# Optimization experiments

Hardware: AMD Instinct MI355X
Metric: run time of the kernel (lower is better)

## Reference

```python
import jax, jax.numpy as jnp
import numpy as np

N, P, D = 128, 256, 256
H, M = 16, 32            # num_heads, head_dim; output_dim = H*M = 512
OUT, HID = H * M, 2048


def setup_inputs() -> dict:
    key = jax.random.key(0)
    ks = jax.random.split(key, 7)
    s = 0.02
    return {
        "x": jax.random.normal(ks[0], (N, P, D), jnp.float32),
        "qkv_temporal": jax.random.normal(ks[1], (3, D, H, M), jnp.float32) * s,
        "qkv_point": jax.random.normal(ks[2], (3, H, M, H, M), jnp.float32) * s,
        "W1": jax.random.normal(ks[3], (OUT, HID), jnp.float32) * s,
        "b1": jnp.zeros((HID,), jnp.float32),
        "W2": jax.random.normal(ks[4], (HID, OUT), jnp.float32) * s,
        "b2": jnp.zeros((OUT,), jnp.float32),
    }


def reference(x, qkv_temporal, qkv_point, W1, b1, W2, b2):
    # ---- temporal attention (over frames i/I, per point j) ----
    qkv = jnp.einsum('wdhm,ijd->whmij', qkv_temporal, x)     # (3,H,M,N,P)
    q, k, v = qkv[0], qkv[1], qkv[2]
    scores = jnp.einsum('hmij,hmIj->hiIj', q, k)             # (H,N,N,P)
    weights = jax.nn.softmax(scores, axis=2)
    # NOTE: label order 'hIij' (positional) matches the original source exactly
    temporal = jnp.einsum('hIij,hmIj->hmij', weights, v)     # (H,M,N,P)
    # ---- point attention (over points j/J, per frame i) ----
    qkv = jnp.einsum('whmHM,HMij->whmij', qkv_point, temporal)  # (3,H,M,N,P)
    q, k, v = qkv[0], qkv[1], qkv[2]
    scores = jnp.einsum('hmij,hmiJ->hijJ', q, k)             # (H,N,P,P)
    weights = jax.nn.softmax(scores, axis=-1)
    pa = jnp.einsum('hijJ,hmiJ->ijhm', weights, v)           # (N,P,H,M)
    pa = pa.reshape(pa.shape[0], pa.shape[1], -1)            # (N,P,H*M)
    # ---- two-layer MLP (no activation, matching the source) ----
    h = pa @ W1 + b1
    return h @ W2 + b2
```

## Files before the change

### kernel.cpp

```cpp
#include <hip/hip_runtime.h>
#include <cstddef>
#include <cstdint>

constexpr int Nf = 128, Pp = 256, Dd = 256, Hh = 16, Mm = 32;
constexpr int OUTC = 512, HID = 2048, C3 = 1536;

typedef short short8 __attribute__((ext_vector_type(8)));
typedef float f32x4 __attribute__((ext_vector_type(4)));

__device__ inline unsigned short f2bf(float f) {
  unsigned u = __float_as_uint(f);
  u += 0x7fffu + ((u >> 16) & 1u);
  return (unsigned short)(u >> 16);
}
__device__ inline unsigned pk2(float a, float b) {
  return (unsigned)f2bf(a) | ((unsigned)f2bf(b) << 16);
}

__global__ __launch_bounds__(256) void conv_x(const float* __restrict__ x,
                                              short* __restrict__ xb) {
  int idx = blockIdx.x * 256 + threadIdx.x;
  const float4* s = (const float4*)x + (size_t)idx * 2;
  float4 a = s[0], c = s[1];
  uint4 o;
  o.x = pk2(a.x, a.y); o.y = pk2(a.z, a.w);
  o.z = pk2(c.x, c.y); o.w = pk2(c.z, c.w);
  ((uint4*)xb)[idx] = o;
}

__global__ __launch_bounds__(256) void transpose_to_bf16(const float* __restrict__ in,
                                                         short* __restrict__ out,
                                                         int R, int C) {
  __shared__ float tile[64 * 65];
  const int t = threadIdx.x;
  const int rb = blockIdx.y * 64, cb = blockIdx.x * 64;
  const size_t sl = (size_t)blockIdx.z * R * C;
#pragma unroll
  for (int u = 0; u < 4; ++u) {
    int r = (t >> 4) + u * 16, c4 = (t & 15) * 4;
    float4 v = *(const float4*)(in + sl + (size_t)(rb + r) * C + cb + c4);
    tile[r * 65 + c4 + 0] = v.x;
    tile[r * 65 + c4 + 1] = v.y;
    tile[r * 65 + c4 + 2] = v.z;
    tile[r * 65 + c4 + 3] = v.w;
  }
  __syncthreads();
#pragma unroll
  for (int u = 0; u < 2; ++u) {
    int id = t + u * 256;
    int n = id >> 3, kg = id & 7;
    float a[8];
#pragma unroll
    for (int q = 0; q < 8; ++q) a[q] = tile[(kg * 8 + q) * 65 + n];
    uint4 o;
    o.x = pk2(a[0], a[1]); o.y = pk2(a[2], a[3]);
    o.z = pk2(a[4], a[5]); o.w = pk2(a[6], a[7]);
    *(uint4*)(out + sl + (size_t)(cb + n) * R + rb + kg * 8) = o;
  }
}

__global__ void repack_b2t(const float* __restrict__ Wp, short* __restrict__ B2t) {
  int idx = blockIdx.x * 256 + threadIdx.x;
  int c = idx >> 9, k = idx & 511;
  int w = c >> 9, h = (c >> 5) & 15, m = c & 31;
  int HH = k >> 5, MM = k & 31;
  B2t[idx] = (short)f2bf(Wp[(((w * Hh + h) * Mm + m) * Hh + HH) * Mm + MM]);
}

__global__ __launch_bounds__(256) void wc_splitk(const short* __restrict__ A,
                                                 const short* __restrict__ Bt,
                                                 float* __restrict__ part) {
  __shared__ short As[128 * 32];
  __shared__ short Bs[128 * 32];
  const int t = threadIdx.x;
  const int wv = t >> 6, ln = t & 63;
  const int wr = wv >> 1, wc = wv & 1;
  const int lr = ln & 15, kq = ln >> 4;
  const int row0 = blockIdx.y * 128, col0 = blockIdx.x * 128;
  const int k0 = blockIdx.z * 256;

  f32x4 acc[4][4];
#pragma unroll
  for (int i = 0; i < 4; ++i)
#pragma unroll
    for (int j = 0; j < 4; ++j) acc[i][j] = {0.f, 0.f, 0.f, 0.f};

  for (int kt = k0; kt < k0 + 256; kt += 32) {
#pragma unroll
    for (int u = 0; u < 2; ++u) {
      int seg = wv * 128 + u * 64 + ln;
      int r = seg >> 2, kg = seg & 3;
      const short* gp = A + (size_t)(row0 + r) * HID + kt + kg * 8;
      __builtin_amdgcn_global_load_lds(
          (const __attribute__((address_space(1))) void*)gp,
          (__attribute__((address_space(3))) void*)&As[(wv * 128 + u * 64) * 8], 16, 0, 0);
    }
#pragma unroll
    for (int u = 0; u < 2; ++u) {
      int seg = wv * 128 + u * 64 + ln;
      int r = seg >> 2, kg = seg & 3;
      const short* gp = Bt + (size_t)(col0 + r) * HID + kt + kg * 8;
      __builtin_amdgcn_global_load_lds(
          (const __attribute__((address_space(1))) void*)gp,
          (__attribute__((address_space(3))) void*)&Bs[(wv * 128 + u * 64) * 8], 16, 0, 0);
    }
    __syncthreads();
    short8 a[4], b[4];
#pragma unroll
    for (int ti = 0; ti < 4; ++ti)
      a[ti] = *(const short8*)&As[(wr * 64 + ti * 16 + lr) * 32 + kq * 8];
#pragma unroll
    for (int tj = 0; tj < 4; ++tj)
      b[tj] = *(const short8*)&Bs[(wc * 64 + tj * 16 + lr) * 32 + kq * 8];
#pragma unroll
    for (int ti = 0; ti < 4; ++ti)
#pragma unroll
      for (int tj = 0; tj < 4; ++tj)
        acc[ti][tj] = __builtin_amdgcn_mfma_f32_16x16x32_bf16(a[ti], b[tj], acc[ti][tj], 0, 0, 0);
    __syncthreads();
  }

#pragma unroll
  for (int tj = 0; tj < 4; ++tj) {
    int gcol = col0 + wc * 64 + tj * 16 + lr;
#pragma unroll
    for (int ti = 0; ti < 4; ++ti)
#pragma unroll
      for (int rg = 0; rg < 4; ++rg) {
        int grow = row0 + wr * 64 + ti * 16 + kq * 4 + rg;
        part[((size_t)blockIdx.z * 512 + grow) * 512 + gcol] = acc[ti][tj][rg];
      }
  }
}

__global__ __launch_bounds__(256) void wc_reduce(const float* __restrict__ part,
                                                 short* __restrict__ Wct) {
  int idx = blockIdx.x * 256 + threadIdx.x;
  float s = 0.f;
#pragma unroll
  for (int z = 0; z < 8; ++z) s += part[(size_t)z * 262144 + idx];
  Wct[idx] = (short)f2bf(s);
}

__global__ __launch_bounds__(256) void bc_partial(const float* __restrict__ b1,
                                                  const float* __restrict__ W2,
                                                  float* __restrict__ part) {
  const int z = blockIdx.x;
  const int t = threadIdx.x;
  float s0 = 0.f, s1 = 0.f;
#pragma unroll
  for (int hh = 0; hh < 32; ++hh) {
    int h = z * 32 + hh;
    float bv = b1[h];
    s0 += bv * W2[(size_t)h * OUTC + t];
    s1 += bv * W2[(size_t)h * OUTC + t + 256];
  }
  part[z * OUTC + t] = s0;
  part[z * OUTC + t + 256] = s1;
}

__global__ __launch_bounds__(256) void bc_finish(const float* __restrict__ part,
                                                 const float* __restrict__ b2,
                                                 float* __restrict__ bc) {
  int o = blockIdx.x * 256 + threadIdx.x;
  float s = b2[o];
#pragma unroll
  for (int z = 0; z < 64; ++z) s += part[z * OUTC + o];
  bc[o] = s;
}

template <int KDIM, int NCOLS, int AMAP, int EPI, int OUTT>
__global__ __launch_bounds__(256) void gemm_mfma(const short* __restrict__ A,
                                                 const short* __restrict__ Bt,
                                                 void* __restrict__ Cv,
                                                 const float* __restrict__ bias,
                                                 int j0, int pshift, int pc) {
  __shared__ __align__(16) short SH[16384];
  const int t = threadIdx.x;
  const int wv = t >> 6, ln = t & 63;
  const int wr = wv >> 1, wc = wv & 1;
  const int lr = ln & 15, kq = ln >> 4;

  constexpr int NBX = NCOLS / 128;
  constexpr int NT = KDIM / 32;
  int lin = blockIdx.y * NBX + blockIdx.x;
  int nblk = gridDim.x * gridDim.y;
  int bx, by;
  if ((nblk & 7) == 0) {
    int per = nblk >> 3;
    int id = (lin & 7) * per + (lin >> 3);
    bx = id % NBX; by = id / NBX;
  } else {
    bx = blockIdx.x; by = blockIdx.y;
  }
  const int row0 = by * 128, col0 = bx * 128;

  const int seg0 = wv * 128 + ln;
  const int seg1 = wv * 128 + 64 + ln;
  const int r0 = seg0 >> 2, r1 = seg1 >> 2;
  const int kg0 = (seg0 & 3) ^ ((r0 >> 1) & 3);
  const int kg1 = (seg1 & 3) ^ ((r1 >> 1) & 3);
  size_t arow0, arow1;
  {
    int rr = row0 + r0;
    if (AMAP == 0)      arow0 = (size_t)rr;
    else if (AMAP == 3) arow0 = (size_t)(((rr & 127) << 8) + (rr >> 7));
    else { int i = rr >> pshift, jj = rr & (pc - 1); arow0 = (size_t)((i << 8) + j0 + jj); }
    rr = row0 + r1;
    if (AMAP == 0)      arow1 = (size_t)rr;
    else if (AMAP == 3) arow1 = (size_t)(((rr & 127) << 8) + (rr >> 7));
    else { int i = rr >> pshift, jj = rr & (pc - 1); arow1 = (size_t)((i << 8) + j0 + jj); }
  }
  const size_t brow0 = (size_t)(col0 + r0), brow1 = (size_t)(col0 + r1);

  auto stage = [&](int buf, int tk) {
    const int kt = tk * 32;
    __builtin_amdgcn_global_load_lds(
        (const __attribute__((address_space(1))) void*)(A + arow0 * KDIM + kt + kg0 * 8),
        (__attribute__((address_space(3))) void*)&SH[buf * 4096 + (wv * 128) * 8], 16, 0, 0);
    __builtin_amdgcn_global_load_lds(
        (const __attribute__((address_space(1))) void*)(A + arow1 * KDIM + kt + kg1 * 8),
        (__attribute__((address_space(3))) void*)&SH[buf * 4096 + (wv * 128 + 64) * 8], 16, 0, 0);
    __builtin_amdgcn_global_load_lds(
        (const __attribute__((address_space(1))) void*)(Bt + brow0 * KDIM + kt + kg0 * 8),
        (__attribute__((address_space(3))) void*)&SH[8192 + buf * 4096 + (wv * 128) * 8], 16, 0, 0);
    __builtin_amdgcn_global_load_lds(
        (const __attribute__((address_space(1))) void*)(Bt + brow1 * KDIM + kt + kg1 * 8),
        (__attribute__((address_space(3))) void*)&SH[8192 + buf * 4096 + (wv * 128 + 64) * 8], 16, 0, 0);
  };

  f32x4 acc[4][4];
#pragma unroll
  for (int i = 0; i < 4; ++i)
#pragma unroll
    for (int j = 0; j < 4; ++j) acc[i][j] = {0.f, 0.f, 0.f, 0.f};

  const int slot = kq ^ ((lr >> 1) & 3);

  stage(0, 0);
  stage(1, 1);
  asm volatile("s_waitcnt vmcnt(4)" ::: "memory");
  __builtin_amdgcn_s_barrier();

  for (int tk = 0; tk < NT; ++tk) {
    const int cur = tk & 1;
    short8 a[4], b[4];
#pragma unroll
    for (int ti = 0; ti < 4; ++ti)
      a[ti] = *(const short8*)&SH[cur * 4096 + (wr * 64 + ti * 16 + lr) * 32 + slot * 8];
#pragma unroll
    for (int tj = 0; tj < 4; ++tj)
      b[tj] = *(const short8*)&SH[8192 + cur * 4096 + (wc * 64 + tj * 16 + lr) * 32 + slot * 8];
    __builtin_amdgcn_sched_barrier(0);
    asm volatile("s_waitcnt lgkmcnt(0)" ::: "memory");
    __builtin_amdgcn_sched_barrier(0);
    if (tk + 1 < NT) {
      __builtin_amdgcn_s_barrier();
      if (tk + 2 < NT) stage(cur, tk + 2);
    }
#pragma unroll
    for (int ti = 0; ti < 4; ++ti)
#pragma unroll
      for (int tj = 0; tj < 4; ++tj)
        acc[ti][tj] = __builtin_amdgcn_mfma_f32_16x16x32_bf16(a[ti], b[tj], acc[ti][tj], 0, 0, 0);
    if (tk + 1 < NT) {
      if (tk + 2 < NT) {
        asm volatile("s_waitcnt vmcnt(4)" ::: "memory");
      } else {
        asm volatile("s_waitcnt vmcnt(0)" ::: "memory");
      }
      __builtin_amdgcn_s_barrier();
      __builtin_amdgcn_sched_barrier(0);
    }
  }

  if (EPI == 0 || EPI == 1) {
#pragma unroll
    for (int tj = 0; tj < 4; ++tj) {
      int gcol = col0 + wc * 64 + tj * 16 + lr;
      float bv = (EPI == 0) ? bias[gcol] : 0.f;
#pragma unroll
      for (int ti = 0; ti < 4; ++ti) {
#pragma unroll
        for (int rg = 0; rg < 4; ++rg) {
          int grow = row0 + wr * 64 + ti * 16 + kq * 4 + rg;
          float val = acc[ti][tj][rg];
          if (EPI == 0) {
            val += bv;
            if (OUTT == 0) ((short*)Cv)[(size_t)grow * NCOLS + gcol] = (short)f2bf(val);
            else           ((float*)Cv)[(size_t)grow * NCOLS + gcol] = val;
          } else {
            int w = gcol >> 9, h = (gcol >> 5) & 15, m = gcol & 31;
            int i = grow >> pshift, jj = grow & (pc - 1);
            size_t addr = (((size_t)(w * Hh + h) * pc + jj) * Nf + i) * Mm + m;
            ((short*)Cv)[addr] = (short)f2bf(val);
          }
        }
      }
    }
  } else {
    __builtin_amdgcn_s_barrier();
#pragma unroll
    for (int ti = 0; ti < 4; ++ti)
#pragma unroll
      for (int tj = 0; tj < 4; ++tj) {
        int c = wc * 64 + tj * 16 + lr;
        int q = c >> 5, m = c & 31;
#pragma unroll
        for (int rg = 0; rg < 4; ++rg) {
          int g = wr * 64 + ti * 16 + kq * 4 + rg;
          SH[q * 4096 + g * 32 + (m ^ ((g & 4) << 2))] = (short)f2bf(acc[ti][tj][rg]);
        }
      }
    __syncthreads();
#pragma unroll
    for (int u = 0; u < 8; ++u) {
      int id = u * 256 + t;
      int q = id >> 9, rem = id & 511, g = rem >> 2, mc = (rem & 3) * 8;
      uint4 v = *(const uint4*)&SH[q * 4096 + g * 32 + (mc ^ ((g & 4) << 2))];
      int gc = col0 + q * 32;
      int w = gc >> 9, h = (gc >> 5) & 15;
      size_t base;
      if (EPI == 3) base = ((size_t)(w * Hh + h) * 256 + (row0 >> 7)) * 4096;
      else          base = (((size_t)(w * Hh + h) * pc + (row0 >> 8)) * 256 + (row0 & 255)) * 32;
      *(uint4*)((short*)Cv + base + g * 32 + mc) = v;
    }
  }
}

__global__ __launch_bounds__(256) void temporal_attn_mfma(const short* __restrict__ T,
                                                          short* __restrict__ At,
                                                          int j0, int jcShift) {
  constexpr int QsO = 0, KsO = 4096, VtO = 8192, WtO = 12544, RsO = 29952;
  __shared__ __align__(16) short lds[30464];
  float* rs = (float*)&lds[RsO];
  const int JC = 1 << jcShift;
  const int h  = blockIdx.x >> jcShift;
  const int jj = blockIdx.x & (JC - 1);
  const int t  = threadIdx.x;
  const int wv = t >> 6, ln = t & 63;
  const int wr = wv >> 1, wc = wv & 1;
  const int lr = ln & 15, kq = ln >> 4;
  const size_t WC = (size_t)(Hh << jcShift) * 4096;
  const short* qb = T + (size_t)(h * JC + jj) * 4096;
  const short* kb = qb + WC;
  const short* vb = qb + 2 * WC;

#pragma unroll
  for (int u = 0; u < 2; ++u) {
    int seg = wv * 2 + u;
    __builtin_amdgcn_global_load_lds(
        (const __attribute__((address_space(1))) void*)(qb + seg * 512 + ln * 8),
        (__attribute__((address_space(3))) void*)&lds[QsO + seg * 512], 16, 0, 0);
    __builtin_amdgcn_global_load_lds(
        (const __attribute__((address_space(1))) void*)(kb + seg * 512 + ln * 8),
        (__attribute__((address_space(3))) void*)&lds[KsO + seg * 512], 16, 0, 0);
  }
#pragma unroll
  for (int u = 0; u < 2; ++u) {
    int idx = t + u * 256;
    int I = idx >> 2, m0 = (idx & 3) * 8;
    uint4 v = *(const uint4*)(vb + idx * 8);
    const short* vs = (const short*)&v;
#pragma unroll
    for (int q = 0; q < 8; ++q) lds[VtO + (m0 + q) * 136 + I] = vs[q];
  }
  __syncthreads();

  short8 af[4], bf[4];
#pragma unroll
  for (int ti = 0; ti < 4; ++ti)
    af[ti] = *(const short8*)&lds[QsO + (wr * 64 + ti * 16 + lr) * 32 + kq * 8];
#pragma unroll
  for (int tj = 0; tj < 4; ++tj)
    bf[tj] = *(const short8*)&lds[KsO + (wc * 64 + tj * 16 + lr) * 32 + kq * 8];
  f32x4 e[4][4];
#pragma unroll
  for (int ti = 0; ti < 4; ++ti)
#pragma unroll
    for (int tj = 0; tj < 4; ++tj) e[ti][tj] = {0.f, 0.f, 0.f, 0.f};
#pragma unroll
  for (int ti = 0; ti < 4; ++ti)
#pragma unroll
    for (int tj = 0; tj < 4; ++tj)
      e[ti][tj] = __builtin_amdgcn_mfma_f32_16x16x32_bf16(af[ti], bf[tj], e[ti][tj], 0, 0, 0);

  float part[4][4];
#pragma unroll
  for (int ti = 0; ti < 4; ++ti)
#pragma unroll
    for (int r = 0; r < 4; ++r) {
      float p = 0.f;
#pragma unroll
      for (int tj = 0; tj < 4; ++tj) {
        float ex = __expf(e[ti][tj][r]);
        e[ti][tj][r] = ex;
        p += ex;
      }
      part[ti][r] = p;
    }
#pragma unroll
  for (int msk = 1; msk <= 8; msk <<= 1)
#pragma unroll
    for (int ti = 0; ti < 4; ++ti)
#pragma unroll
      for (int r = 0; r < 4; ++r)
        part[ti][r] += __shfl_xor(part[ti][r], msk, 64);
  if (lr == 0) {
#pragma unroll
    for (int ti = 0; ti < 4; ++ti)
#pragma unroll
      for (int r = 0; r < 4; ++r)
        rs[wc * 128 + wr * 64 + ti * 16 + kq * 4 + r] = part[ti][r];
  }
  __syncthreads();

#pragma unroll
  for (int ti = 0; ti < 4; ++ti) {
#pragma unroll
    for (int r = 0; r < 4; ++r) {
      int I = wr * 64 + ti * 16 + kq * 4 + r;
      float inv = 1.f / (rs[I] + rs[128 + I]);
#pragma unroll
      for (int tj = 0; tj < 4; ++tj) e[ti][tj][r] *= inv;
    }
#pragma unroll
    for (int tj = 0; tj < 4; ++tj) {
      int i = wc * 64 + tj * 16 + lr;
      int Ib = wr * 64 + ti * 16 + kq * 4;
      uint2 pk;
      pk.x = pk2(e[ti][tj][0], e[ti][tj][1]);
      pk.y = pk2(e[ti][tj][2], e[ti][tj][3]);
      *(uint2*)&lds[WtO + i * 136 + Ib] = pk;
    }
  }
  __syncthreads();

  f32x4 o[2][2];
#pragma unroll
  for (int tr = 0; tr < 2; ++tr)
#pragma unroll
    for (int tm = 0; tm < 2; ++tm) o[tr][tm] = {0.f, 0.f, 0.f, 0.f};
#pragma unroll
  for (int ks = 0; ks < 4; ++ks) {
    short8 ea[2], vf[2];
#pragma unroll
    for (int tr = 0; tr < 2; ++tr)
      ea[tr] = *(const short8*)&lds[WtO + (wv * 32 + tr * 16 + lr) * 136 + ks * 32 + kq * 8];
#pragma unroll
    for (int tm = 0; tm < 2; ++tm)
      vf[tm] = *(const short8*)&lds[VtO + (tm * 16 + lr) * 136 + ks * 32 + kq * 8];
#pragma unroll
    for (int tr = 0; tr < 2; ++tr)
#pragma unroll
      for (int tm = 0; tm < 2; ++tm)
        o[tr][tm] = __builtin_amdgcn_mfma_f32_16x16x32_bf16(ea[tr], vf[tm], o[tr][tm], 0, 0, 0);
  }
#pragma unroll
  for (int tr = 0; tr < 2; ++tr)
#pragma unroll
    for (int tm = 0; tm < 2; ++tm)
#pragma unroll
      for (int r = 0; r < 4; ++r) {
        int row = wv * 32 + tr * 16 + kq * 4 + r;
        lds[row * 40 + tm * 16 + lr] = (short)f2bf(o[tr][tm][r]);
      }
  __syncthreads();
#pragma unroll
  for (int u = 0; u < 2; ++u) {
    int idx = t + u * 256;
    int i = idx >> 2, mg = idx & 3;
    uint4 vv = *(const uint4*)&lds[i * 40 + mg * 8];
    *(uint4*)(At + ((size_t)(i * Pp + j0 + jj) * OUTC + h * 32 + mg * 8)) = vv;
  }
}

__global__ __launch_bounds__(256) void point_attn_mfma(const short* __restrict__ P,
                                                       short* __restrict__ PA,
                                                       int icShift) {
  constexpr int QsO = 0, KsO = 4096, VtO = 8192, EO = 12544, CsO = 29952;
  __shared__ __align__(16) short lds[30720];
  float* cs    = (float*)&lds[CsO];
  float* denom = cs + 256;
  const int IC = 1 << icShift;
  const int bx = blockIdx.x;
  const int h    = bx >> (icShift + 1);
  const int rem  = bx & ((IC << 1) - 1);
  const int ii   = rem >> 1;
  const int half = rem & 1;
  const int t  = threadIdx.x;
  const int wv = t >> 6, ln = t & 63;
  const int wr = wv >> 1, wc = wv & 1;
  const int lr = ln & 15, kq = ln >> 4;
  const size_t WC = (size_t)(Hh << icShift) * 8192;
  const short* qb = P + (size_t)(h * IC + ii) * 8192 + half * 4096;
  const short* kb = P + WC + (size_t)(h * IC + ii) * 8192;
  const short* vb = kb + WC;

  f32x4 o[2][2];
#pragma unroll
  for (int tr = 0; tr < 2; ++tr)
#pragma unroll
    for (int tm = 0; tm < 2; ++tm) o[tr][tm] = {0.f, 0.f, 0.f, 0.f};

  for (int chunk = 0; chunk < 2; ++chunk) {
    const int Jb = chunk * 128;
    if (chunk) __syncthreads();
#pragma unroll
    for (int u = 0; u < 2; ++u) {
      int seg = wv * 2 + u;
      __builtin_amdgcn_global_load_lds(
          (const __attribute__((address_space(1))) void*)(kb + Jb * 32 + seg * 512 + ln * 8),
          (__attribute__((address_space(3))) void*)&lds[KsO + seg * 512], 16, 0, 0);
    }
    if (chunk == 0) {
#pragma unroll
      for (int u = 0; u < 2; ++u) {
        int seg = wv * 2 + u;
        __builtin_amdgcn_global_load_lds(
            (const __attribute__((address_space(1))) void*)(qb + seg * 512 + ln * 8),
            (__attribute__((address_space(3))) void*)&lds[QsO + seg * 512], 16, 0, 0);
      }
      if (t < 128) denom[t] = 0.f;
    }
#pragma unroll
    for (int u = 0; u < 2; ++u) {
      int idx = t + u * 256;
      int Jl = idx >> 2, m0 = (idx & 3) * 8;
      uint4 v = *(const uint4*)(vb + Jb * 32 + idx * 8);
      const short* vs = (const short*)&v;
#pragma unroll
      for (int q = 0; q < 8; ++q) lds[VtO + (m0 + q) * 136 + Jl] = vs[q];
    }
    __syncthreads();

    short8 af[4], bf[4];
#pragma unroll
    for (int ti = 0; ti < 4; ++ti)
      af[ti] = *(const short8*)&lds[KsO + (wr * 64 + ti * 16 + lr) * 32 + kq * 8];
#pragma unroll
    for (int tj = 0; tj < 4; ++tj)
      bf[tj] = *(const short8*)&lds[QsO + (wc * 64 + tj * 16 + lr) * 32 + kq * 8];
    f32x4 e[4][4];
#pragma unroll
    for (int ti = 0; ti < 4; ++ti)
#pragma unroll
      for (int tj = 0; tj < 4; ++tj) e[ti][tj] = {0.f, 0.f, 0.f, 0.f};
#pragma unroll
    for (int ti = 0; ti < 4; ++ti)
#pragma unroll
      for (int tj = 0; tj < 4; ++tj)
        e[ti][tj] = __builtin_amdgcn_mfma_f32_16x16x32_bf16(af[ti], bf[tj], e[ti][tj], 0, 0, 0);

    float cp[4] = {0.f, 0.f, 0.f, 0.f};
#pragma unroll
    for (int ti = 0; ti < 4; ++ti)
#pragma unroll
      for (int tj = 0; tj < 4; ++tj)
#pragma unroll
        for (int r = 0; r < 4; ++r) {
          float ex = __expf(e[ti][tj][r]);
          e[ti][tj][r] = ex;
          cp[tj] += ex;
        }
#pragma unroll
    for (int tj = 0; tj < 4; ++tj) {
      cp[tj] += __shfl_xor(cp[tj], 16, 64);
      cp[tj] += __shfl_xor(cp[tj], 32, 64);
    }
    if (kq == 0) {
#pragma unroll
      for (int tj = 0; tj < 4; ++tj)
        cs[wr * 128 + wc * 64 + tj * 16 + lr] = cp[tj];
    }
#pragma unroll
    for (int ti = 0; ti < 4; ++ti)
#pragma unroll
      for (int tj = 0; tj < 4; ++tj) {
        int j  = wc * 64 + tj * 16 + lr;
        int Jl = wr * 64 + ti * 16 + kq * 4;
        uint2 pk;
        pk.x = pk2(e[ti][tj][0], e[ti][tj][1]);
        pk.y = pk2(e[ti][tj][2], e[ti][tj][3]);
        *(uint2*)&lds[EO + j * 136 + Jl] = pk;
      }
    __syncthreads();
    if (t < 128) denom[t] += cs[t] + cs[128 + t];

#pragma unroll
    for (int ks = 0; ks < 4; ++ks) {
      short8 ea[2], vf[2];
#pragma unroll
      for (int tr = 0; tr < 2; ++tr)
        ea[tr] = *(const short8*)&lds[EO + (wv * 32 + tr * 16 + lr) * 136 + ks * 32 + kq * 8];
#pragma unroll
      for (int tm = 0; tm < 2; ++tm)
        vf[tm] = *(const short8*)&lds[VtO + (tm * 16 + lr) * 136 + ks * 32 + kq * 8];
#pragma unroll
      for (int tr = 0; tr < 2; ++tr)
#pragma unroll
        for (int tm = 0; tm < 2; ++tm)
          o[tr][tm] = __builtin_amdgcn_mfma_f32_16x16x32_bf16(ea[tr], vf[tm], o[tr][tm], 0, 0, 0);
    }
  }
  __syncthreads();

#pragma unroll
  for (int tr = 0; tr < 2; ++tr)
#pragma unroll
    for (int r = 0; r < 4; ++r) {
      int row = wv * 32 + tr * 16 + kq * 4 + r;
      float rinv = 1.f / denom[row];
#pragma unroll
      for (int tm = 0; tm < 2; ++tm)
        lds[row * 40 + tm * 16 + lr] = (short)f2bf(o[tr][tm][r] * rinv);
    }
  __syncthreads();
#pragma unroll
  for (int u = 0; u < 2; ++u) {
    int idx = t + u * 256;
    int jl = idx >> 2, mg = idx & 3;
    uint4 vv = *(const uint4*)&lds[jl * 40 + mg * 8];
    *(uint4*)(PA + ((size_t)(ii * Pp + half * 128 + jl) * OUTC + h * 32 + mg * 8)) = vv;
  }
}

extern "C" void kernel_launch(void* const* d_in, const int* in_sizes, int n_in,
                              void* d_out, int out_size, void* d_ws, size_t ws_size,
                              hipStream_t stream) {
  const float* x  = (const float*)d_in[0];
  const float* Wt = (const float*)d_in[1];
  const float* Wp = (const float*)d_in[2];
  const float* W1 = (const float*)d_in[3];
  const float* b1 = (const float*)d_in[4];
  const float* W2 = (const float*)d_in[5];
  const float* b2 = (const float*)d_in[6];
  float* out = (float*)d_out;
  short* ws  = (short*)d_ws;

  const size_t fixedH = 8388608 + 16777216 + 393216 + 786432 + 1048576 + 1048576
                      + 262144 + 1024 + 4194304 + 65536;
  size_t availH = ws_size / 2;
  size_t chF; int JC, IC;
  if      (availH >= fixedH + 50331648) { chF = 50331648; JC = 256; IC = 128; }
  else if (availH >= fixedH + 12582912) { chF = 12582912; JC = 64;  IC = 32;  }
  else if (availH >= fixedH + 6291456)  { chF = 6291456;  JC = 32;  IC = 16;  }
  else                                  { chF = 3145728;  JC = 16;  IC = 8;   }
  short* CH  = ws;
  short* xbf = CH + chF;
  short* At  = xbf + 8388608;
  short* B1t = At + 16777216;
  short* B2t = B1t + 393216;
  short* W1b = B2t + 786432;
  short* W2t = W1b + 1048576;
  short* Wct = W2t + 1048576;
  float* bcF   = (float*)(Wct + 262144);
  float* partF = (float*)(Wct + 262144 + 1024);
  float* bcP   = (float*)(Wct + 262144 + 1024 + 4194304);
  const int jcS = __builtin_ctz((unsigned)JC);
  const int icS = __builtin_ctz((unsigned)IC);

  conv_x<<<4096, 256, 0, stream>>>(x, xbf);
  conv_x<<<512, 256, 0, stream>>>(W1, W1b);
  transpose_to_bf16<<<dim3(8, 4, 3), 256, 0, stream>>>(Wt, B1t, 256, 512);
  repack_b2t<<<3072, 256, 0, stream>>>(Wp, B2t);
  transpose_to_bf16<<<dim3(8, 32, 1), 256, 0, stream>>>(W2, W2t, 2048, 512);

  wc_splitk<<<dim3(4, 4, 8), 256, 0, stream>>>(W2t, W1b, partF);
  wc_reduce<<<1024, 256, 0, stream>>>(partF, Wct);
  bc_partial<<<64, 256, 0, stream>>>(b1, W2, bcP);
  bc_finish<<<2, 256, 0, stream>>>(bcP, b2, bcF);

  if (JC == 256) {
    gemm_mfma<256, 1536, 3, 3, 0><<<dim3(12, 256), 256, 0, stream>>>(xbf, B1t, CH, nullptr, 0, 0, 256);
    temporal_attn_mfma<<<Hh * 256, 256, 0, stream>>>(CH, At, 0, 8);
    gemm_mfma<512, 1536, 0, 2, 0><<<dim3(12, 256), 256, 0, stream>>>(At, B2t, CH, nullptr, 0, 0, 128);
    point_attn_mfma<<<Hh * 128 * 2, 256, 0, stream>>>(CH, At, 7);
  } else {
    for (int j0 = 0; j0 < Pp; j0 += JC) {
      gemm_mfma<256, 1536, 1, 1, 0><<<dim3(12, JC), 256, 0, stream>>>(xbf, B1t, CH, nullptr, j0, jcS, JC);
      temporal_attn_mfma<<<Hh * JC, 256, 0, stream>>>(CH, At, j0, jcS);
    }
    for (int i0 = 0; i0 < Nf; i0 += IC) {
      short* Arows = At + (size_t)i0 * Pp * OUTC;
      gemm_mfma<512, 1536, 0, 2, 0><<<dim3(12, IC * 2), 256, 0, stream>>>(Arows, B2t, CH, nullptr, 0, 0, IC);
      point_attn_mfma<<<Hh * IC * 2, 256, 0, stream>>>(CH, Arows, icS);
    }
  }

  gemm_mfma<512, 512, 0, 0, 1><<<dim3(4, 256), 256, 0, stream>>>(At, Wct, out, bcF, 0, 0, 0);
}
```

Before: 368.2 us.

## Swizzle Q/K LDS layout, rotate V transpose stores, use hardware bf16 pack

Q and K tiles are now loaded into LDS with an XOR-swizzled 16-byte slot per row, and the MFMA fragment reads use the matching swizzled slot. The aim is to remove LDS bank conflicts on the short8 reads in both attention kernels. The V transpose stores are rotated per lane group so the four groups write different rows in the same cycle, which targets conflicts in the scattered 2-byte stores. The software float-to-bf16 rounding in pk2 is replaced with the v_cvt_pk_bf16_f32 instruction, which risks small rounding or NaN-handling differences and depends on the instruction being available on this target.

```diff
diff --git a/kernel.cpp b/kernel.cpp
--- a/kernel.cpp
+++ b/kernel.cpp
@@ -14,7 +14,9 @@
   return (unsigned short)(u >> 16);
 }
 __device__ inline unsigned pk2(float a, float b) {
-  return (unsigned)f2bf(a) | ((unsigned)f2bf(b) << 16);
+  unsigned r;
+  asm("v_cvt_pk_bf16_f32 %0, %1, %2" : "=v"(r) : "v"(a), "v"(b));
+  return r;
 }
 
 __global__ __launch_bounds__(256) void conv_x(const float* __restrict__ x,
@@ -346,34 +348,45 @@
   const short* kb = qb + WC;
   const short* vb = qb + 2 * WC;
 
+  const int lnoff = (ln >> 2) * 32 + (((ln & 3) ^ ((ln >> 3) & 3)) * 8);
+  const int qkslot = (kq ^ ((lr >> 1) & 3)) * 8;
+
 #pragma unroll
   for (int u = 0; u < 2; ++u) {
     int seg = wv * 2 + u;
     __builtin_amdgcn_global_load_lds(
-        (const __attribute__((address_space(1))) void*)(qb + seg * 512 + ln * 8),
+        (const __attribute__((address_space(1))) void*)(qb + seg * 512 + lnoff),
         (__attribute__((address_space(3))) void*)&lds[QsO + seg * 512], 16, 0, 0);
     __builtin_amdgcn_global_load_lds(
-        (const __attribute__((address_space(1))) void*)(kb + seg * 512 + ln * 8),
+        (const __attribute__((address_space(1))) void*)(kb + seg * 512 + lnoff),
         (__attribute__((address_space(3))) void*)&lds[KsO + seg * 512], 16, 0, 0);
   }
 #pragma unroll
   for (int u = 0; u < 2; ++u) {
     int idx = t + u * 256;
-    int I = idx >> 2, m0 = (idx & 3) * 8;
+    int I = idx >> 2, g = idx & 3;
     uint4 v = *(const uint4*)(vb + idx * 8);
-    const short* vs = (const short*)&v;
-#pragma unroll
-    for (int q = 0; q < 8; ++q) lds[VtO + (m0 + q) * 136 + I] = vs[q];
+    unsigned w0 = v.x, w1 = v.y, w2 = v.z, w3 = v.w;
+    if (g & 1) { unsigned tp = w0; w0 = w1; w1 = w2; w2 = w3; w3 = tp; }
+    if (g & 2) { unsigned t0 = w0, t1 = w1; w0 = w2; w1 = w3; w2 = t0; w3 = t1; }
+    const unsigned wa[4] = {w0, w1, w2, w3};
+    int m0 = g * 8, g2 = g * 2;
+#pragma unroll
+    for (int k = 0; k < 4; ++k) {
+      int q = (2 * k + g2) & 7;
+      lds[VtO + (m0 + q) * 136 + I]     = (short)(wa[k] & 0xffffu);
+      lds[VtO + (m0 + q + 1) * 136 + I] = (short)(wa[k] >> 16);
+    }
   }
   __syncthreads();
 
   short8 af[4], bf[4];
 #pragma unroll
   for (int ti = 0; ti < 4; ++ti)
-    af[ti] = *(const short8*)&lds[QsO + (wr * 64 + ti * 16 + lr) * 32 + kq * 8];
+    af[ti] = *(const short8*)&lds[QsO + (wr * 64 + ti * 16 + lr) * 32 + qkslot];
 #pragma unroll
   for (int tj = 0; tj < 4; ++tj)
-    bf[tj] = *(const short8*)&lds[KsO + (wc * 64 + tj * 16 + lr) * 32 + kq * 8];
+    bf[tj] = *(const short8*)&lds[KsO + (wc * 64 + tj * 16 + lr) * 32 + qkslot];
   f32x4 e[4][4];
 #pragma unroll
   for (int ti = 0; ti < 4; ++ti)
@@ -497,6 +510,9 @@
   const short* kb = P + WC + (size_t)(h * IC + ii) * 8192;
   const short* vb = kb + WC;
 
+  const int lnoff = (ln >> 2) * 32 + (((ln & 3) ^ ((ln >> 3) & 3)) * 8);
+  const int qkslot = (kq ^ ((lr >> 1) & 3)) * 8;
+
   f32x4 o[2][2];
 #pragma unroll
   for (int tr = 0; tr < 2; ++tr)
@@ -510,7 +526,7 @@
     for (int u = 0; u < 2; ++u) {
       int seg = wv * 2 + u;
       __builtin_amdgcn_global_load_lds(
-          (const __attribute__((address_space(1))) void*)(kb + Jb * 32 + seg * 512 + ln * 8),
+          (const __attribute__((address_space(1))) void*)(kb + Jb * 32 + seg * 512 + lnoff),
           (__attribute__((address_space(3))) void*)&lds[KsO + seg * 512], 16, 0, 0);
     }
     if (chunk == 0) {
@@ -518,7 +534,7 @@
       for (int u = 0; u < 2; ++u) {
         int seg = wv * 2 + u;
         __builtin_amdgcn_global_load_lds(
-            (const __attribute__((address_space(1))) void*)(qb + seg * 512 + ln * 8),
+            (const __attribute__((address_space(1))) void*)(qb + seg * 512 + lnoff),
             (__attribute__((address_space(3))) void*)&lds[QsO + seg * 512], 16, 0, 0);
       }
       if (t < 128) denom[t] = 0.f;
@@ -526,21 +542,29 @@
 #pragma unroll
     for (int u = 0; u < 2; ++u) {
       int idx = t + u * 256;
-      int Jl = idx >> 2, m0 = (idx & 3) * 8;
+      int Jl = idx >> 2, g = idx & 3;
       uint4 v = *(const uint4*)(vb + Jb * 32 + idx * 8);
-      const short* vs = (const short*)&v;
-#pragma unroll
-      for (int q = 0; q < 8; ++q) lds[VtO + (m0 + q) * 136 + Jl] = vs[q];
+      unsigned w0 = v.x, w1 = v.y, w2 = v.z, w3 = v.w;
+      if (g & 1) { unsigned tp = w0; w0 = w1; w1 = w2; w2 = w3; w3 = tp; }
+      if (g & 2) { unsigned t0 = w0, t1 = w1; w0 = w2; w1 = w3; w2 = t0; w3 = t1; }
+      const unsigned wa[4] = {w0, w1, w2, w3};
+      int m0 = g * 8, g2 = g * 2;
+#pragma unroll
+      for (int k = 0; k < 4; ++k) {
+        int q = (2 * k + g2) & 7;
+        lds[VtO + (m0 + q) * 136 + Jl]     = (short)(wa[k] & 0xffffu);
+        lds[VtO + (m0 + q + 1) * 136 + Jl] = (short)(wa[k] >> 16);
+      }
     }
     __syncthreads();
 
     short8 af[4], bf[4];
 #pragma unroll
     for (int ti = 0; ti < 4; ++ti)
-      af[ti] = *(const short8*)&lds[KsO + (wr * 64 + ti * 16 + lr) * 32 + kq * 8];
+      af[ti] = *(const short8*)&lds[KsO + (wr * 64 + ti * 16 + lr) * 32 + qkslot];
 #pragma unroll
     for (int tj = 0; tj < 4; ++tj)
-      bf[tj] = *(const short8*)&lds[QsO + (wc * 64 + tj * 16 + lr) * 32 + kq * 8];
+      bf[tj] = *(const short8*)&lds[QsO + (wc * 64 + tj * 16 + lr) * 32 + qkslot];
     f32x4 e[4][4];
 #pragma unroll
     for (int ti = 0; ti < 4; ++ti)
```

Result: no change. 370.0 us (+0.5%).
